# Kernel optimization log

Measured on AMD Instinct MI355X. Metric: run time of the kernel, lower is better.

## Reference

```python
import jax, jax.numpy as jnp
import numpy as np

B, T, E, H = 4, 2048, 1024, 16
D = E // H
SCALE = 1.0 / np.sqrt(D)


def setup_inputs() -> dict:
    key = jax.random.key(0)
    ks = jax.random.split(key, 5)
    s_in = 1.0 / np.sqrt(E)
    return {
        "x": jax.random.normal(ks[0], (B, T, E), dtype=jnp.float32),
        "W_qkv": jax.random.normal(ks[1], (E, 3 * E), dtype=jnp.float32) * s_in,
        "b_qkv": jax.random.normal(ks[2], (3 * E,), dtype=jnp.float32) * 0.02,
        "W_proj": jax.random.normal(ks[3], (E, E), dtype=jnp.float32) * s_in,
        "b_proj": jax.random.normal(ks[4], (E,), dtype=jnp.float32) * 0.02,
    }


def reference(x, W_qkv, b_qkv, W_proj, b_proj):
    Bx, Tx, _ = x.shape
    qkv = x @ W_qkv + b_qkv                      # [B, T, 3E]
    q, k, v = jnp.split(qkv, 3, axis=2)
    q = q.reshape(Bx, Tx, H, D)
    k = k.reshape(Bx, Tx, H, D)
    v = v.reshape(Bx, Tx, H, D)
    # scores [B, H, T, T]
    a = SCALE * jnp.einsum("bthd,bshd->bhts", q, k)
    causal = jnp.tril(jnp.ones((Tx, Tx), dtype=bool))
    a = jnp.where(causal, a, -jnp.inf)
    a = jax.nn.softmax(a, axis=-1)
    y = jnp.einsum("bhts,bshd->bthd", a, v).reshape(Bx, Tx, E)
    return y @ W_proj + b_proj
```

## Files before the change

### kernel.cpp

```cpp
#include <hip/hip_runtime.h>
#include <math.h>

#define Bn 4
#define Tn 2048
#define En 1024
#define Hn 16
#define Dn 64
#define RS2 (2 * En)
#define QSCALE 0.18033688f
#define SMAX 16.0f

typedef __attribute__((ext_vector_type(8))) short bfrag;
typedef __attribute__((ext_vector_type(4))) short sfrag4;
typedef __attribute__((ext_vector_type(4))) float ffrag;

__device__ __forceinline__ unsigned short f2bf(float f) {
    union { float f; unsigned int u; } v; v.f = f;
    unsigned int r = v.u + 0x7fffu + ((v.u >> 16) & 1u);
    return (unsigned short)(r >> 16);
}
__device__ __forceinline__ unsigned short f2bf_fast(float f) {
    union { float f; unsigned int u; } v; v.f = f;
    return (unsigned short)((v.u + 0x8000u) >> 16);
}

__device__ __forceinline__ void glds16(const unsigned short* g, unsigned short* l) {
    __builtin_amdgcn_global_load_lds(
        (const __attribute__((address_space(1))) unsigned int*)g,
        (__attribute__((address_space(3))) unsigned int*)l, 16, 0, 0);
}

#define VMCNT0() asm volatile("s_waitcnt vmcnt(0)" ::: "memory")
#define BAR()    __builtin_amdgcn_s_barrier()

__global__ __launch_bounds__(256) void f2bf_vec(const float* __restrict__ in,
                                                unsigned short* __restrict__ out, int n) {
    int i = (blockIdx.x * 256 + threadIdx.x) * 4;
    if (i >= n) return;
    float4 v = *(const float4*)(in + i);
    ushort4 o;
    o.x = f2bf(v.x); o.y = f2bf(v.y); o.z = f2bf(v.z); o.w = f2bf(v.w);
    *(ushort4*)(out + i) = o;
}

__global__ __launch_bounds__(256) void transpose_f2bf(const float* __restrict__ W,
                                                      unsigned short* __restrict__ Wt,
                                                      int K, int N) {
    __shared__ float s[64][65];
    const int kt = blockIdx.y * 64, nt = blockIdx.x * 64;
    const int tx = threadIdx.x & 15, ty = threadIdx.x >> 4;
#pragma unroll
    for (int i = 0; i < 4; ++i) {
        float4 v = *(const float4*)&W[(size_t)(kt + ty + i * 16) * N + nt + tx * 4];
        s[ty + i * 16][tx * 4 + 0] = v.x;
        s[ty + i * 16][tx * 4 + 1] = v.y;
        s[ty + i * 16][tx * 4 + 2] = v.z;
        s[ty + i * 16][tx * 4 + 3] = v.w;
    }
    __syncthreads();
#pragma unroll
    for (int i = 0; i < 4; ++i) {
        const int n = ty + i * 16;
        ushort4 o;
        o.x = f2bf(s[tx * 4 + 0][n]);
        o.y = f2bf(s[tx * 4 + 1][n]);
        o.z = f2bf(s[tx * 4 + 2][n]);
        o.w = f2bf(s[tx * 4 + 3][n]);
        *(ushort4*)&Wt[(size_t)(nt + n) * K + kt + tx * 4] = o;
    }
}

template <int OUT_BF16, int VSPLIT>
__global__ __launch_bounds__(256) void gemm_nt_mfma(
    const unsigned short* __restrict__ A, const unsigned short* __restrict__ Bt,
    const float* __restrict__ bias, void* __restrict__ Cv, int ldc,
    unsigned short* __restrict__ vt, int vstart,
    int M, int N, int K, int qcols, int gx)
{
    __shared__ __attribute__((aligned(16))) unsigned short As[2][128 * 64];
    __shared__ __attribute__((aligned(16))) unsigned short Bs[2][128 * 64];

    const int t = threadIdx.x;
    const int w = t >> 6, l = t & 63;
    const int wmt = (w & 1) * 4, wnt = (w >> 1) * 4;
    const int nl = l & 15, lq = l >> 4;
    const int r8 = l >> 3, c8 = l & 7;
    const int cs8 = c8 ^ r8;

    const int flat = blockIdx.x;
    const int xcd = flat & 7;
    const int g = flat >> 3;
    const int bx = g % gx;
    const int by = xcd * 8 + g / gx;
    const int m0 = by * 128, n0 = bx * 128;

    ffrag acc[4][4];
#pragma unroll
    for (int i = 0; i < 4; ++i)
#pragma unroll
        for (int j = 0; j < 4; ++j)
#pragma unroll
            for (int r = 0; r < 4; ++r) acc[i][j][r] = 0.f;

    const unsigned short* Ag = A  + (size_t)(m0 + r8) * K + cs8 * 8;
    const unsigned short* Bg = Bt + (size_t)(n0 + r8) * K + cs8 * 8;

    const int iters = K >> 6;

#pragma unroll
    for (int r = 0; r < 4; ++r) {
        const int i = w * 4 + r;
        glds16(Ag + (size_t)(i * 8) * K, &As[0][i * 512 + l * 8]);
        glds16(Bg + (size_t)(i * 8) * K, &Bs[0][i * 512 + l * 8]);
    }
    __syncthreads();

#pragma unroll 1
    for (int it = 0; it < iters; ++it) {
        const int cur = it & 1;
        if (it + 1 < iters) {
            const int kn = (it + 1) << 6;
#pragma unroll
            for (int r = 0; r < 4; ++r) {
                const int i = w * 4 + r;
                glds16(Ag + (size_t)(i * 8) * K + kn, &As[cur ^ 1][i * 512 + l * 8]);
                glds16(Bg + (size_t)(i * 8) * K + kn, &Bs[cur ^ 1][i * 512 + l * 8]);
            }
        }
#pragma unroll
        for (int ks = 0; ks < 2; ++ks) {
            bfrag af[4], bf[4];
#pragma unroll
            for (int i = 0; i < 4; ++i) {
                const int pos = ((ks * 4 + lq) ^ (nl & 7)) << 3;
                af[i] = *(const bfrag*)&As[cur][((wmt + i) * 16 + nl) * 64 + pos];
                bf[i] = *(const bfrag*)&Bs[cur][((wnt + i) * 16 + nl) * 64 + pos];
            }
#pragma unroll
            for (int i = 0; i < 4; ++i)
#pragma unroll
                for (int j = 0; j < 4; ++j)
                    acc[i][j] = __builtin_amdgcn_mfma_f32_16x16x32_bf16(af[i], bf[j], acc[i][j], 0, 0, 0);
        }
        VMCNT0();
        BAR();
    }

    const int orow = lq * 4, ocol = nl;
#pragma unroll
    for (int i = 0; i < 4; ++i) {
        const int gm = m0 + (wmt + i) * 16 + orow;
#pragma unroll
        for (int j = 0; j < 4; ++j) {
            const int gn = n0 + (wnt + j) * 16 + ocol;
            const float bs = bias[gn];
            if (VSPLIT && gn >= vstart) {
                const int vc = gn - vstart;
                const int b  = gm / Tn;
                const int tt = gm - b * Tn;
                ushort4 o;
                o.x = f2bf(acc[i][j][0] + bs);
                o.y = f2bf(acc[i][j][1] + bs);
                o.z = f2bf(acc[i][j][2] + bs);
                o.w = f2bf(acc[i][j][3] + bs);
                *(ushort4*)&vt[(size_t)(b * Hn * Dn + vc) * Tn + tt] = o;
            } else {
                const float sc = (qcols && gn < qcols) ? QSCALE : 1.f;
#pragma unroll
                for (int r = 0; r < 4; ++r) {
                    const float vv = (acc[i][j][r] + bs) * sc;
                    if (OUT_BF16)
                        ((unsigned short*)Cv)[(size_t)(gm + r) * ldc + gn] = f2bf(vv);
                    else
                        ((float*)Cv)[(size_t)(gm + r) * ldc + gn] = vv;
                }
            }
        }
    }
}

__global__ __launch_bounds__(256, 4) void attn_mfma(
    const unsigned short* __restrict__ qkv,
    const unsigned short* __restrict__ vtg,
    unsigned short* __restrict__ yattn)
{
    __shared__ __attribute__((aligned(16))) unsigned short KT[128 * 64];
    __shared__ __attribute__((aligned(16))) unsigned short VT[64 * 128];

    const int t = threadIdx.x;
    const int w = t >> 6, l = t & 63;
    const int nl = l & 15, lq = l >> 4;
    const int flat = blockIdx.x;
    const int bh = flat & 63;
    const int qp = flat >> 6;
    const int b = bh >> 4, h = bh & 15;

    const unsigned short* qbase = qkv + (size_t)(b * Tn) * RS2 + h * Dn;
    const unsigned short* kbase = qbase + En;
    const unsigned short* vbase = vtg + (size_t)(bh * Dn) * Tn;
    unsigned short* yb = yattn + (size_t)(b * Tn) * En + h * Dn;

#pragma unroll 1
    for (int phase = 0; phase < 2; ++phase) {
        const int qt = phase ? (31 - qp) : qp;
        const int rowb = qt * 64 + w * 16;
        const int jmax = qt >> 1;
        const int qrow = rowb + nl;

        bfrag qf[2];
#pragma unroll
        for (int ks = 0; ks < 2; ++ks)
            qf[ks] = *(const bfrag*)(qbase + (size_t)(rowb + nl) * RS2 + ks * 32 + lq * 8);

        ffrag Oa[4];
        float li = 0.f;
#pragma unroll
        for (int dt = 0; dt < 4; ++dt)
#pragma unroll
            for (int r = 0; r < 4; ++r) Oa[dt][r] = 0.f;

        for (int j = 0; j <= jmax; ++j) {
            const int k0 = j << 7;
            __syncthreads();
#pragma unroll
            for (int r = 0; r < 4; ++r) {
                const int i = w * 4 + r;
                glds16(kbase + (size_t)(k0 + i * 8 + (l >> 3)) * RS2 + (((l & 7) ^ (l >> 3)) << 3),
                       &KT[i * 512 + l * 8]);
            }
#pragma unroll
            for (int r = 0; r < 4; ++r) {
                const int i = w * 4 + r;
                const int key = ((i & 3) << 2) + (l >> 4);
                glds16(vbase + (size_t)(i * 4 + (l >> 4)) * Tn + k0 + (((l & 15) ^ key) << 3),
                       &VT[i * 512 + l * 8]);
            }
            __syncthreads();

            bfrag pf[4];
#pragma unroll
            for (int cs = 0; cs < 4; ++cs) {
                const int n0 = cs * 2, n1 = cs * 2 + 1;
                const int pos0 = (lq ^ (nl & 7)) << 3;
                const int pos1 = ((4 + lq) ^ (nl & 7)) << 3;
                bfrag ka0 = *(const bfrag*)&KT[(n0 * 16 + nl) * 64 + pos0];
                bfrag kb0 = *(const bfrag*)&KT[(n0 * 16 + nl) * 64 + pos1];
                bfrag ka1 = *(const bfrag*)&KT[(n1 * 16 + nl) * 64 + pos0];
                bfrag kb1 = *(const bfrag*)&KT[(n1 * 16 + nl) * 64 + pos1];
                ffrag z0, z1;
#pragma unroll
                for (int r = 0; r < 4; ++r) { z0[r] = -SMAX; z1[r] = -SMAX; }
                __builtin_amdgcn_s_setprio(1);
                z0 = __builtin_amdgcn_mfma_f32_16x16x32_bf16(ka0, qf[0], z0, 0, 0, 0);
                z0 = __builtin_amdgcn_mfma_f32_16x16x32_bf16(kb0, qf[1], z0, 0, 0, 0);
                z1 = __builtin_amdgcn_mfma_f32_16x16x32_bf16(ka1, qf[0], z1, 0, 0, 0);
                z1 = __builtin_amdgcn_mfma_f32_16x16x32_bf16(kb1, qf[1], z1, 0, 0, 0);
                __builtin_amdgcn_s_setprio(0);
                if (j == jmax) {
#pragma unroll
                    for (int r = 0; r < 4; ++r) {
                        if (k0 + n0 * 16 + lq * 4 + r > qrow) z0[r] = -INFINITY;
                        if (k0 + n1 * 16 + lq * 4 + r > qrow) z1[r] = -INFINITY;
                    }
                }
#pragma unroll
                for (int r = 0; r < 4; ++r) {
                    const float p0 = __builtin_amdgcn_exp2f(z0[r]);
                    const float p1 = __builtin_amdgcn_exp2f(z1[r]);
                    li += p0;
                    li += p1;
                    pf[cs][r]     = (short)f2bf_fast(p0);
                    pf[cs][4 + r] = (short)f2bf_fast(p1);
                }
            }

            __builtin_amdgcn_s_setprio(1);
#pragma unroll
            for (int cs = 0; cs < 4; ++cs) {
#pragma unroll
                for (int dt = 0; dt < 4; ++dt) {
                    const int d = dt * 16 + nl;
                    const int base = d * 128 + ((lq & 1) << 2);
                    const int cA = (((cs << 2) + (lq >> 1)) ^ nl) << 3;
                    const int cB = (((cs << 2) + 2 + (lq >> 1)) ^ nl) << 3;
                    sfrag4 va = *(const sfrag4*)&VT[base + cA];
                    sfrag4 vb = *(const sfrag4*)&VT[base + cB];
                    bfrag vf = __builtin_shufflevector(va, vb, 0, 1, 2, 3, 4, 5, 6, 7);
                    Oa[dt] = __builtin_amdgcn_mfma_f32_16x16x32_bf16(pf[cs], vf, Oa[dt], 0, 0, 0);
                }
            }
            __builtin_amdgcn_s_setprio(0);
        }

        li += __shfl_xor(li, 16, 64);
        li += __shfl_xor(li, 32, 64);
#pragma unroll
        for (int r = 0; r < 4; ++r) {
            const float lr = __shfl(li, lq * 4 + r, 64);
            const float inv = 1.f / lr;
            const int row = rowb + lq * 4 + r;
#pragma unroll
            for (int dt = 0; dt < 4; ++dt)
                yb[(size_t)row * En + dt * 16 + nl] = f2bf(Oa[dt][r] * inv);
        }
    }
}

extern "C" void kernel_launch(void* const* d_in, const int* in_sizes, int n_in,
                              void* d_out, int out_size, void* d_ws, size_t ws_size,
                              hipStream_t stream)
{
    const float* x      = (const float*)d_in[0];
    const float* W_qkv  = (const float*)d_in[1];
    const float* b_qkv  = (const float*)d_in[2];
    const float* W_proj = (const float*)d_in[3];
    const float* b_proj = (const float*)d_in[4];
    float* out = (float*)d_out;

    const int M = Bn * Tn;
    char* ws = (char*)d_ws;
    unsigned short* xb   = (unsigned short*)ws; ws += (size_t)M * En * 2;
    unsigned short* Wqt  = (unsigned short*)ws; ws += (size_t)3 * En * En * 2;
    unsigned short* Wpt  = (unsigned short*)ws; ws += (size_t)En * En * 2;
    unsigned short* qkb  = (unsigned short*)ws; ws += (size_t)M * 2 * En * 2;
    unsigned short* vtg  = (unsigned short*)ws; ws += (size_t)M * En * 2;
    unsigned short* yb   = (unsigned short*)ws;

    f2bf_vec<<<(M * En / 4 + 255) / 256, 256, 0, stream>>>(x, xb, M * En);
    transpose_f2bf<<<dim3(3 * En / 64, En / 64), 256, 0, stream>>>(W_qkv, Wqt, En, 3 * En);
    transpose_f2bf<<<dim3(En / 64, En / 64), 256, 0, stream>>>(W_proj, Wpt, En, En);

    gemm_nt_mfma<1, 1><<<dim3((3 * En / 128) * (M / 128)), 256, 0, stream>>>(
        xb, Wqt, b_qkv, qkb, 2 * En, vtg, 2 * En, M, 3 * En, En, En, 3 * En / 128);

    attn_mfma<<<dim3(1024), 256, 0, stream>>>(qkb, vtg, yb);

    gemm_nt_mfma<0, 0><<<dim3((En / 128) * (M / 128)), 256, 0, stream>>>(
        yb, Wpt, b_proj, out, En, nullptr, 1 << 30, M, En, En, 0, En / 128);
}
```

Measured before the change: 247.8 us.

## Process 128 query rows per attention block to reuse each K/V tile twice

Each attention block now handles two 64-row query sub-tiles against every staged 128-key K/V tile in LDS. This halves the K/V global loads and LDS staging per query row, and the grid shrinks from 1024 to 512 blocks. The causal pairing of tiles (qp with 15-qp) keeps the work per block balanced. In exchange, register pressure roughly doubles for the Q fragments, the score tiles and the accumulators, and the minimum-occupancy launch bound is dropped, so fewer waves run per CU to hide latency.

```diff
diff --git a/kernel.cpp b/kernel.cpp
--- a/kernel.cpp
+++ b/kernel.cpp
@@ -179,7 +179,7 @@
     }
 }
 
-__global__ __launch_bounds__(256, 4) void attn_mfma(
+__global__ __launch_bounds__(256) void attn_mfma(
     const unsigned short* __restrict__ qkv,
     const unsigned short* __restrict__ vtg,
     unsigned short* __restrict__ yattn)
@@ -202,22 +202,27 @@
 
 #pragma unroll 1
     for (int phase = 0; phase < 2; ++phase) {
-        const int qt = phase ? (31 - qp) : qp;
-        const int rowb = qt * 64 + w * 16;
-        const int jmax = qt >> 1;
-        const int qrow = rowb + nl;
-
-        bfrag qf[2];
-#pragma unroll
-        for (int ks = 0; ks < 2; ++ks)
-            qf[ks] = *(const bfrag*)(qbase + (size_t)(rowb + nl) * RS2 + ks * 32 + lq * 8);
-
-        ffrag Oa[4];
-        float li = 0.f;
-#pragma unroll
-        for (int dt = 0; dt < 4; ++dt)
-#pragma unroll
-            for (int r = 0; r < 4; ++r) Oa[dt][r] = 0.f;
+        const int qt = phase ? (15 - qp) : qp;
+        const int rowb = qt * 128 + w * 16;
+        const int jmax = qt;
+
+        bfrag qf[2][2];
+#pragma unroll
+        for (int sub = 0; sub < 2; ++sub)
+#pragma unroll
+            for (int ks = 0; ks < 2; ++ks)
+                qf[sub][ks] = *(const bfrag*)(qbase + (size_t)(rowb + sub * 64 + nl) * RS2 + ks * 32 + lq * 8);
+
+        ffrag Oa[2][4];
+        float li[2];
+#pragma unroll
+        for (int sub = 0; sub < 2; ++sub) {
+            li[sub] = 0.f;
+#pragma unroll
+            for (int dt = 0; dt < 4; ++dt)
+#pragma unroll
+                for (int r = 0; r < 4; ++r) Oa[sub][dt][r] = 0.f;
+        }
 
         for (int j = 0; j <= jmax; ++j) {
             const int k0 = j << 7;
@@ -237,7 +242,7 @@
             }
             __syncthreads();
 
-            bfrag pf[4];
+            bfrag pf[2][4];
 #pragma unroll
             for (int cs = 0; cs < 4; ++cs) {
                 const int n0 = cs * 2, n1 = cs * 2 + 1;
@@ -247,30 +252,34 @@
                 bfrag kb0 = *(const bfrag*)&KT[(n0 * 16 + nl) * 64 + pos1];
                 bfrag ka1 = *(const bfrag*)&KT[(n1 * 16 + nl) * 64 + pos0];
                 bfrag kb1 = *(const bfrag*)&KT[(n1 * 16 + nl) * 64 + pos1];
-                ffrag z0, z1;
-#pragma unroll
-                for (int r = 0; r < 4; ++r) { z0[r] = -SMAX; z1[r] = -SMAX; }
-                __builtin_amdgcn_s_setprio(1);
-                z0 = __builtin_amdgcn_mfma_f32_16x16x32_bf16(ka0, qf[0], z0, 0, 0, 0);
-                z0 = __builtin_amdgcn_mfma_f32_16x16x32_bf16(kb0, qf[1], z0, 0, 0, 0);
-                z1 = __builtin_amdgcn_mfma_f32_16x16x32_bf16(ka1, qf[0], z1, 0, 0, 0);
-                z1 = __builtin_amdgcn_mfma_f32_16x16x32_bf16(kb1, qf[1], z1, 0, 0, 0);
-                __builtin_amdgcn_s_setprio(0);
-                if (j == jmax) {
+#pragma unroll
+                for (int sub = 0; sub < 2; ++sub) {
+                    const int qrow = rowb + sub * 64 + nl;
+                    ffrag z0, z1;
+#pragma unroll
+                    for (int r = 0; r < 4; ++r) { z0[r] = -SMAX; z1[r] = -SMAX; }
+                    __builtin_amdgcn_s_setprio(1);
+                    z0 = __builtin_amdgcn_mfma_f32_16x16x32_bf16(ka0, qf[sub][0], z0, 0, 0, 0);
+                    z0 = __builtin_amdgcn_mfma_f32_16x16x32_bf16(kb0, qf[sub][1], z0, 0, 0, 0);
+                    z1 = __builtin_amdgcn_mfma_f32_16x16x32_bf16(ka1, qf[sub][0], z1, 0, 0, 0);
+                    z1 = __builtin_amdgcn_mfma_f32_16x16x32_bf16(kb1, qf[sub][1], z1, 0, 0, 0);
+                    __builtin_amdgcn_s_setprio(0);
+                    if (j == jmax) {
+#pragma unroll
+                        for (int r = 0; r < 4; ++r) {
+                            if (k0 + n0 * 16 + lq * 4 + r > qrow) z0[r] = -INFINITY;
+                            if (k0 + n1 * 16 + lq * 4 + r > qrow) z1[r] = -INFINITY;
+                        }
+                    }
 #pragma unroll
                     for (int r = 0; r < 4; ++r) {
-                        if (k0 + n0 * 16 + lq * 4 + r > qrow) z0[r] = -INFINITY;
-                        if (k0 + n1 * 16 + lq * 4 + r > qrow) z1[r] = -INFINITY;
+                        const float p0 = __builtin_amdgcn_exp2f(z0[r]);
+                        const float p1 = __builtin_amdgcn_exp2f(z1[r]);
+                        li[sub] += p0;
+                        li[sub] += p1;
+                        pf[sub][cs][r]     = (short)f2bf_fast(p0);
+                        pf[sub][cs][4 + r] = (short)f2bf_fast(p1);
                     }
-                }
-#pragma unroll
-                for (int r = 0; r < 4; ++r) {
-                    const float p0 = __builtin_amdgcn_exp2f(z0[r]);
-                    const float p1 = __builtin_amdgcn_exp2f(z1[r]);
-                    li += p0;
-                    li += p1;
-                    pf[cs][r]     = (short)f2bf_fast(p0);
-                    pf[cs][4 + r] = (short)f2bf_fast(p1);
                 }
             }
 
@@ -286,22 +295,27 @@
                     sfrag4 va = *(const sfrag4*)&VT[base + cA];
                     sfrag4 vb = *(const sfrag4*)&VT[base + cB];
                     bfrag vf = __builtin_shufflevector(va, vb, 0, 1, 2, 3, 4, 5, 6, 7);
-                    Oa[dt] = __builtin_amdgcn_mfma_f32_16x16x32_bf16(pf[cs], vf, Oa[dt], 0, 0, 0);
+                    Oa[0][dt] = __builtin_amdgcn_mfma_f32_16x16x32_bf16(pf[0][cs], vf, Oa[0][dt], 0, 0, 0);
+                    Oa[1][dt] = __builtin_amdgcn_mfma_f32_16x16x32_bf16(pf[1][cs], vf, Oa[1][dt], 0, 0, 0);
                 }
             }
             __builtin_amdgcn_s_setprio(0);
         }
 
-        li += __shfl_xor(li, 16, 64);
-        li += __shfl_xor(li, 32, 64);
-#pragma unroll
-        for (int r = 0; r < 4; ++r) {
-            const float lr = __shfl(li, lq * 4 + r, 64);
-            const float inv = 1.f / lr;
-            const int row = rowb + lq * 4 + r;
-#pragma unroll
-            for (int dt = 0; dt < 4; ++dt)
-                yb[(size_t)row * En + dt * 16 + nl] = f2bf(Oa[dt][r] * inv);
+#pragma unroll
+        for (int sub = 0; sub < 2; ++sub) {
+            float ls = li[sub];
+            ls += __shfl_xor(ls, 16, 64);
+            ls += __shfl_xor(ls, 32, 64);
+#pragma unroll
+            for (int r = 0; r < 4; ++r) {
+                const float lr = __shfl(ls, lq * 4 + r, 64);
+                const float inv = 1.f / lr;
+                const int row = rowb + sub * 64 + lq * 4 + r;
+#pragma unroll
+                for (int dt = 0; dt < 4; ++dt)
+                    yb[(size_t)row * En + dt * 16 + nl] = f2bf(Oa[sub][dt][r] * inv);
+            }
         }
     }
 }
@@ -333,7 +347,7 @@
     gemm_nt_mfma<1, 1><<<dim3((3 * En / 128) * (M / 128)), 256, 0, stream>>>(
         xb, Wqt, b_qkv, qkb, 2 * En, vtg, 2 * En, M, 3 * En, En, En, 3 * En / 128);
 
-    attn_mfma<<<dim3(1024), 256, 0, stream>>>(qkb, vtg, yb);
+    attn_mfma<<<dim3(512), 256, 0, stream>>>(qkb, vtg, yb);
 
     gemm_nt_mfma<0, 0><<<dim3((En / 128) * (M / 128)), 256, 0, stream>>>(
         yb, Wpt, b_proj, out, En, nullptr, 1 << 30, M, En, En, 0, En / 128);
```

After: 246.0 us. No clear change (-0.7%).
